# Kernel tuning notes

Measured on AMD Instinct MI355X. Metric: run time of the kernel, lower is better.

Reference implementation:

```python
import jax, jax.numpy as jnp
import numpy as np

EPS = 1e-6

def setup_inputs() -> dict:
    key = jax.random.key(0)
    k1, k2 = jax.random.split(key)
    shape = (20, 1, 128, 128, 128)
    # BCE requires x strictly in (0,1); keep away from endpoints like a sigmoid output.
    x = jax.random.uniform(k1, shape, dtype=jnp.float32, minval=EPS, maxval=1.0 - EPS)
    y = jax.random.uniform(k2, shape, dtype=jnp.float32, minval=0.0, maxval=1.0)
    return {"x": x, "y": y}

def reference(x, y):
    # binary_cross_entropy (mean reduction); torch clamps log terms at -100
    log_x = jnp.clip(jnp.log(x), -100.0)
    log_1mx = jnp.clip(jnp.log1p(-x), -100.0)
    mseloss = -jnp.mean(y * log_x + (1.0 - y) * log_1mx)

    # threshold prediction at 0.5 -> {0,1}; truncate target to int (floor toward 0)
    xb = jnp.where(x > 0.5, 1, 0)              # int
    yb = y.astype(jnp.int32)                   # astype(int) truncation

    B = x.shape[0]  # loop is over range(20); batch == 20
    por_pred = jnp.mean((xb == 0).astype(jnp.float32).reshape(B, -1), axis=1)
    por_true = jnp.mean((yb == 0).astype(jnp.float32).reshape(B, -1), axis=1)
    PORE = jnp.mean((por_pred - por_true) ** 2)  # sum over 20 samples / 20

    return (PORE + mseloss, PORE)
```

## Files before the change

kernel.cpp:

```cpp
#include <hip/hip_runtime.h>

#define NBATCH 20
#define ELEMS_PER_BATCH (128 * 128 * 128)
#define BLOCKS_PER_BATCH 128
#define THREADS 256
#define V4_PER_THREAD 16
#define NPART (NBATCH * BLOCKS_PER_BATCH)

#define LN2 0.69314718055994530942
#define LOG2_CLAMP (-144.26950408889634f)

__global__ __launch_bounds__(THREADS) void partial_kernel(
    const float* __restrict__ x, const float* __restrict__ y,
    float* __restrict__ bce_part, int* __restrict__ pred_part,
    int* __restrict__ true_part) {
  const int b   = blockIdx.y;
  const int seg = blockIdx.x;
  const int tid = threadIdx.x;

  const long base4 = (long)b * (ELEMS_PER_BATCH / 4) +
                     (long)seg * (THREADS * V4_PER_THREAD);
  const float4* __restrict__ x4 = (const float4*)x;
  const float4* __restrict__ y4 = (const float4*)y;

  float bce2 = 0.0f;
  int pc = 0, tc = 0;

#pragma unroll
  for (int k = 0; k < V4_PER_THREAD; ++k) {
    const long idx = base4 + (long)k * THREADS + tid;
    const float4 xv = x4[idx];
    const float4 yv = y4[idx];

#pragma unroll
    for (int c = 0; c < 4; ++c) {
      const float xx = (c == 0) ? xv.x : (c == 1) ? xv.y : (c == 2) ? xv.z : xv.w;
      const float yy = (c == 0) ? yv.x : (c == 1) ? yv.y : (c == 2) ? yv.z : yv.w;
      const float lx = fmaxf(__builtin_amdgcn_logf(xx),        LOG2_CLAMP);
      const float l1 = fmaxf(__builtin_amdgcn_logf(1.0f - xx), LOG2_CLAMP);
      bce2 += l1 + yy * (lx - l1);
      pc += (xx <= 0.5f);
      tc += (yy < 1.0f);
    }
  }

  __shared__ float sb[THREADS];
  __shared__ int   sp[THREADS];
  __shared__ int   st[THREADS];
  sb[tid] = bce2; sp[tid] = pc; st[tid] = tc;
  __syncthreads();
#pragma unroll
  for (int s = THREADS / 2; s > 0; s >>= 1) {
    if (tid < s) {
      sb[tid] += sb[tid + s];
      sp[tid] += sp[tid + s];
      st[tid] += st[tid + s];
    }
    __syncthreads();
  }
  if (tid == 0) {
    const int o = b * BLOCKS_PER_BATCH + seg;
    bce_part[o]  = (float)(sb[0] * LN2);
    pred_part[o] = sp[0];
    true_part[o] = st[0];
  }
}

__global__ __launch_bounds__(THREADS) void final_kernel(
    const float* __restrict__ bce_part, const int* __restrict__ pred_part,
    const int* __restrict__ true_part, float* __restrict__ out) {
  const int tid = threadIdx.x;
  __shared__ double sred[THREADS];
  __shared__ float  spor[NBATCH];

  double local = 0.0;
  for (int i = tid; i < NPART; i += THREADS) local += (double)bce_part[i];
  sred[tid] = local;
  __syncthreads();
#pragma unroll
  for (int s = THREADS / 2; s > 0; s >>= 1) {
    if (tid < s) sred[tid] += sred[tid + s];
    __syncthreads();
  }

  if (tid < NBATCH) {
    int pc = 0, tc = 0;
    for (int k = 0; k < BLOCKS_PER_BATCH; ++k) {
      pc += pred_part[tid * BLOCKS_PER_BATCH + k];
      tc += true_part[tid * BLOCKS_PER_BATCH + k];
    }
    const float pp = (float)pc / (float)ELEMS_PER_BATCH;
    const float pt = (float)tc / (float)ELEMS_PER_BATCH;
    const float d = pp - pt;
    spor[tid] = d * d;
  }
  __syncthreads();

  if (tid == 0) {
    float pore_sum = 0.0f;
#pragma unroll
    for (int b = 0; b < NBATCH; ++b) pore_sum += spor[b];
    const float pore = pore_sum / (float)NBATCH;
    const double total = (double)NBATCH * (double)ELEMS_PER_BATCH;
    const float mse = (float)(-(sred[0] / total));
    out[0] = pore + mse;
    out[1] = pore;
  }
}

extern "C" void kernel_launch(void* const* d_in, const int* in_sizes, int n_in,
                              void* d_out, int out_size, void* d_ws, size_t ws_size,
                              hipStream_t stream) {
  const float* x = (const float*)d_in[0];
  const float* y = (const float*)d_in[1];
  float* out = (float*)d_out;

  float* bce_part  = (float*)d_ws;
  int*   pred_part = (int*)(bce_part + NPART);
  int*   true_part = pred_part + NPART;

  dim3 grid(BLOCKS_PER_BATCH, NBATCH);
  partial_kernel<<<grid, THREADS, 0, stream>>>(x, y, bce_part, pred_part, true_part);
  final_kernel<<<1, THREADS, 0, stream>>>(bce_part, pred_part, true_part, out);
}
```

Baseline: 338.4 us.

## Stream inputs through LDS with async global_load_lds ring-buffer pipeline

Replaces direct float4 global loads with asynchronous global-to-LDS copies in a per-wave four-slot ring, issuing loads three stages ahead and gating each stage with explicit vmcnt waits. The accumulator is also split into four independent partial sums to shorten dependency chains. The intent is to keep memory requests in flight while computing logs. The risk is that it bounds outstanding loads compared with the fully unrolled register loads and adds LDS round-trips.

```diff
diff --git a/kernel.cpp b/kernel.cpp
--- a/kernel.cpp
+++ b/kernel.cpp
@@ -1,53 +1,91 @@
 #include <hip/hip_runtime.h>
 
 #define NBATCH 20
-#define ELEMS_PER_BATCH (128 * 128 * 128)
+#define EPB (128 * 128 * 128)
 #define BLOCKS_PER_BATCH 128
 #define THREADS 256
-#define V4_PER_THREAD 16
+#define NSTAGE 16
+#define NSLOT 4
 #define NPART (NBATCH * BLOCKS_PER_BATCH)
 
 #define LN2 0.69314718055994530942
 #define LOG2_CLAMP (-144.26950408889634f)
 
+#define WAITVM(n) __builtin_amdgcn_s_waitcnt(0xF70 | ((n) & 0xF) | (((n) & 0x30) << 10))
+
+typedef const __attribute__((address_space(1))) void* gas1_t;
+typedef __attribute__((address_space(3))) void* las3_t;
+#define GLD_LDS16(gp, lp) \
+  __builtin_amdgcn_global_load_lds((gas1_t)(const void*)(gp), (las3_t)(void*)(lp), 16, 0, 0)
+
 __global__ __launch_bounds__(THREADS) void partial_kernel(
     const float* __restrict__ x, const float* __restrict__ y,
     float* __restrict__ bce_part, int* __restrict__ pred_part,
     int* __restrict__ true_part) {
-  const int b   = blockIdx.y;
-  const int seg = blockIdx.x;
-  const int tid = threadIdx.x;
+  __shared__ float4 xs[4][NSLOT][64];
+  __shared__ float4 ys[4][NSLOT][64];
+  __shared__ float  sb[THREADS];
+  __shared__ int    sp[THREADS];
+  __shared__ int    st[THREADS];
 
-  const long base4 = (long)b * (ELEMS_PER_BATCH / 4) +
-                     (long)seg * (THREADS * V4_PER_THREAD);
+  const int b    = blockIdx.y;
+  const int seg  = blockIdx.x;
+  const int tid  = threadIdx.x;
+  const int wave = tid >> 6;
+  const int lane = tid & 63;
+
+  const long base4 = (long)b * (EPB / 4) + (long)seg * (THREADS * NSTAGE);
   const float4* __restrict__ x4 = (const float4*)x;
   const float4* __restrict__ y4 = (const float4*)y;
+  const long wbase = base4 + (long)wave * 64 + lane;
 
-  float bce2 = 0.0f;
+#pragma unroll
+  for (int s = 0; s < NSLOT - 1; ++s) {
+    GLD_LDS16(x4 + wbase + (long)s * THREADS, &xs[wave][s][0]);
+    GLD_LDS16(y4 + wbase + (long)s * THREADS, &ys[wave][s][0]);
+  }
+
+  float bce0 = 0.0f, bce1 = 0.0f, bce2 = 0.0f, bce3 = 0.0f;
   int pc = 0, tc = 0;
 
-#pragma unroll
-  for (int k = 0; k < V4_PER_THREAD; ++k) {
-    const long idx = base4 + (long)k * THREADS + tid;
-    const float4 xv = x4[idx];
-    const float4 yv = y4[idx];
+#define STAGE(S)                                                               \
+  do {                                                                         \
+    if ((S) + NSLOT - 1 < NSTAGE) {                                            \
+      GLD_LDS16(x4 + wbase + (long)((S) + 3) * THREADS,                        \
+                &xs[wave][((S) + 3) & 3][0]);                                  \
+      GLD_LDS16(y4 + wbase + (long)((S) + 3) * THREADS,                        \
+                &ys[wave][((S) + 3) & 3][0]);                                  \
+    }                                                                          \
+    WAITVM((2 * (NSTAGE - 1 - (S)) < 6) ? 2 * (NSTAGE - 1 - (S)) : 6);         \
+    __builtin_amdgcn_sched_barrier(0);                                         \
+    {                                                                          \
+      const float4 xv = xs[wave][(S) & 3][lane];                               \
+      const float4 yv = ys[wave][(S) & 3][lane];                               \
+      _Pragma("unroll") for (int c = 0; c < 4; ++c) {                          \
+        const float xx = (c == 0) ? xv.x : (c == 1) ? xv.y                     \
+                                  : (c == 2) ? xv.z : xv.w;                    \
+        const float yy = (c == 0) ? yv.x : (c == 1) ? yv.y                     \
+                                  : (c == 2) ? yv.z : yv.w;                    \
+        const float lx = fmaxf(__builtin_amdgcn_logf(xx),        LOG2_CLAMP);  \
+        const float l1 = fmaxf(__builtin_amdgcn_logf(1.0f - xx), LOG2_CLAMP);  \
+        const float t  = l1 + yy * (lx - l1);                                  \
+        if (c == 0) bce0 += t; else if (c == 1) bce1 += t;                     \
+        else if (c == 2) bce2 += t; else bce3 += t;                            \
+        pc += (xx <= 0.5f);                                                    \
+        tc += (yy < 1.0f);                                                     \
+      }                                                                        \
+    }                                                                          \
+  } while (0)
 
-#pragma unroll
-    for (int c = 0; c < 4; ++c) {
-      const float xx = (c == 0) ? xv.x : (c == 1) ? xv.y : (c == 2) ? xv.z : xv.w;
-      const float yy = (c == 0) ? yv.x : (c == 1) ? yv.y : (c == 2) ? yv.z : yv.w;
-      const float lx = fmaxf(__builtin_amdgcn_logf(xx),        LOG2_CLAMP);
-      const float l1 = fmaxf(__builtin_amdgcn_logf(1.0f - xx), LOG2_CLAMP);
-      bce2 += l1 + yy * (lx - l1);
-      pc += (xx <= 0.5f);
-      tc += (yy < 1.0f);
-    }
-  }
+  STAGE(0);  STAGE(1);  STAGE(2);  STAGE(3);
+  STAGE(4);  STAGE(5);  STAGE(6);  STAGE(7);
+  STAGE(8);  STAGE(9);  STAGE(10); STAGE(11);
+  STAGE(12); STAGE(13); STAGE(14); STAGE(15);
+#undef STAGE
 
-  __shared__ float sb[THREADS];
-  __shared__ int   sp[THREADS];
-  __shared__ int   st[THREADS];
-  sb[tid] = bce2; sp[tid] = pc; st[tid] = tc;
+  const float bce = (bce0 + bce1) + (bce2 + bce3);
+
+  sb[tid] = bce; sp[tid] = pc; st[tid] = tc;
   __syncthreads();
 #pragma unroll
   for (int s = THREADS / 2; s > 0; s >>= 1) {
@@ -89,8 +127,8 @@
       pc += pred_part[tid * BLOCKS_PER_BATCH + k];
       tc += true_part[tid * BLOCKS_PER_BATCH + k];
     }
-    const float pp = (float)pc / (float)ELEMS_PER_BATCH;
-    const float pt = (float)tc / (float)ELEMS_PER_BATCH;
+    const float pp = (float)pc / (float)EPB;
+    const float pt = (float)tc / (float)EPB;
     const float d = pp - pt;
     spor[tid] = d * d;
   }
@@ -99,9 +137,9 @@
   if (tid == 0) {
     float pore_sum = 0.0f;
 #pragma unroll
-    for (int b = 0; b < NBATCH; ++b) pore_sum += spor[b];
+    for (int bb = 0; bb < NBATCH; ++bb) pore_sum += spor[bb];
     const float pore = pore_sum / (float)NBATCH;
-    const double total = (double)NBATCH * (double)ELEMS_PER_BATCH;
+    const double total = (double)NBATCH * (double)EPB;
     const float mse = (float)(-(sred[0] / total));
     out[0] = pore + mse;
     out[1] = pore;
```

Result: no change. 339.1 us (+0.2%).
